# Kernel tuning notes

Measured on AMD Instinct MI355X. Metric: run time of the kernel, lower is better.

## Reference

```python
import jax, jax.numpy as jnp
import numpy as np

N_NODES = 50000
N_EDGES = 800000
IN_FEATS = 256
OUT_FEATS = 64


def setup_inputs() -> dict:
    key = jax.random.key(0)
    k1, k2, k3, k4 = jax.random.split(key, 4)
    feat = jax.random.normal(k1, (N_NODES, IN_FEATS), dtype=jnp.float32)
    src = jax.random.randint(k2, (N_EDGES,), 0, N_NODES, dtype=jnp.int32)
    dst = jax.random.randint(k3, (N_EDGES,), 0, N_NODES, dtype=jnp.int32)
    # Glorot-uniform like DGL's GraphConv weight init
    limit = float(np.sqrt(6.0 / (IN_FEATS + OUT_FEATS)))
    W = jax.random.uniform(k4, (IN_FEATS, OUT_FEATS), dtype=jnp.float32,
                           minval=-limit, maxval=limit)
    b = jnp.zeros((OUT_FEATS,), dtype=jnp.float32)
    return {"feat": feat, "src": src, "dst": dst, "W": W, "b": b}


def reference(feat, src, dst, W, b):
    n = feat.shape[0]
    ones = jnp.ones_like(src, dtype=feat.dtype)
    out_deg = jax.ops.segment_sum(ones, src, num_segments=n)
    in_deg = jax.ops.segment_sum(ones, dst, num_segments=n)
    # norm='both': deg^{-1/2}, degrees clamped to min 1 (allow_zero_in_degree)
    norm_src = jax.lax.rsqrt(jnp.maximum(out_deg, 1.0))   # [N]
    norm_dst = jax.lax.rsqrt(jnp.maximum(in_deg, 1.0))    # [N]
    # in_feats > out_feats -> apply weight before aggregation (DGL fast path)
    h = (feat * norm_src[:, None]) @ W                    # [N, out]
    agg = jax.ops.segment_sum(h[src], dst, num_segments=n)  # SpMM: sum messages at dst
    rst = agg * norm_dst[:, None] + b
    return jax.nn.sigmoid(rst)
```

## Files before the change

### kernel.cpp

```cpp
#include <hip/hip_runtime.h>
#include <hip/hip_bf16.h>
#include <math.h>

#define N_NODES 50000
#define N_EDGES 800000
#define IN_F 256
#define OUT_F 64

#define BKT 256
#define NB 196
#define CAP 6144
#define PARTA_BLOCKS 400
#define EPB (N_EDGES / PARTA_BLOCKS)
#define GEMM_BM 32
#define GEMM_BLOCKS 782

typedef __attribute__((ext_vector_type(8))) short bf16x8;
typedef __attribute__((ext_vector_type(4))) float f32x4;

__device__ __forceinline__ ushort f2bf(float x) {
    __hip_bfloat16 b = __float2bfloat16(x);
    return *reinterpret_cast<ushort*>(&b);
}
__device__ __forceinline__ float bf_lo(uint v) { return __uint_as_float(v << 16); }
__device__ __forceinline__ float bf_hi(uint v) { return __uint_as_float(v & 0xffff0000u); }

__global__ __launch_bounds__(256) void prep_kernel(int* __restrict__ bcnt,
                                                   const float* __restrict__ W,
                                                   ushort* __restrict__ Wpk) {
    const int tid = threadIdx.x;
    if (blockIdx.x == 0) {
        for (int i = tid; i < 2 * NB; i += 256) bcnt[i] = 0;
    } else {
        const int gid = (blockIdx.x - 1) * 256 + tid;
        const int lane = gid & 63;
        const int ct = (gid >> 6) & 3;
        const int step = gid >> 8;
        const int kg = lane >> 4;
        const int n = lane & 15;
        const float* base = W + (size_t)(step * 32 + kg * 8) * OUT_F + ct * 16 + n;
        union { ushort u[8]; uint4 v; } pk;
        #pragma unroll
        for (int j = 0; j < 8; ++j) pk.u[j] = f2bf(base[(size_t)j * OUT_F]);
        ((uint4*)Wpk)[gid] = pk.v;
    }
}

__global__ __launch_bounds__(512) void fused_kernel(const int* __restrict__ src,
                                                    const int* __restrict__ dst,
                                                    int* __restrict__ bcntD,
                                                    int* __restrict__ bcntS,
                                                    uint* __restrict__ pairsD,
                                                    ushort* __restrict__ srcloc,
                                                    const float* __restrict__ feat,
                                                    const ushort* __restrict__ Wpk,
                                                    ushort* __restrict__ h) {
    __shared__ __align__(16) char smem[65536];
    const int bi = blockIdx.x;
    const int tid = threadIdx.x;

    if (bi < 2 * PARTA_BLOCKS && (bi & 1)) {
        int2* ed      = (int2*)smem;
        uint* stgD    = (uint*)(smem + 16000);
        int* lcntD    = (int*)(smem + 24000);
        int* lcntS    = (int*)(smem + 25024);
        int* ldofD    = (int*)(smem + 26048);
        int* ldofS    = (int*)(smem + 27072);
        int* lbaseD   = (int*)(smem + 28096);
        int* lbaseS   = (int*)(smem + 28880);
        int* wtotD    = (int*)(smem + 29664);
        int* wtotS    = (int*)(smem + 29680);
        ushort* stgS  = (ushort*)(smem + 29696);
        const int id = bi >> 1;
        const int n4 = EPB / 4;

        for (int i = tid; i < 256; i += 512) { lcntD[i] = 0; lcntS[i] = 0; }
        __syncthreads();

        const int4* t4 = (const int4*)(dst + (size_t)id * EPB);
        const int4* s4 = (const int4*)(src + (size_t)id * EPB);
        for (int i = tid; i < n4; i += 512) {
            const int4 d = t4[i];
            const int4 s = s4[i];
            ed[4 * i + 0] = (int2){d.x, s.x};
            ed[4 * i + 1] = (int2){d.y, s.y};
            ed[4 * i + 2] = (int2){d.z, s.z};
            ed[4 * i + 3] = (int2){d.w, s.w};
            atomicAdd(&lcntD[d.x >> 8], 1); atomicAdd(&lcntS[s.x >> 8], 1);
            atomicAdd(&lcntD[d.y >> 8], 1); atomicAdd(&lcntS[s.y >> 8], 1);
            atomicAdd(&lcntD[d.z >> 8], 1); atomicAdd(&lcntS[s.z >> 8], 1);
            atomicAdd(&lcntD[d.w >> 8], 1); atomicAdd(&lcntS[s.w >> 8], 1);
        }
        __syncthreads();

        for (int i = tid; i < NB; i += 512) {
            const int cD = lcntD[i];
            lbaseD[i] = cD ? atomicAdd(&bcntD[i], cD) : 0;
            const int cS = lcntS[i];
            lbaseS[i] = cS ? atomicAdd(&bcntS[i], cS) : 0;
        }

        if (tid < 256) {
            const int lane = tid & 63;
            const int wave = tid >> 6;
            const int vD = lcntD[tid], vS = lcntS[tid];
            int iD = vD, iS = vS;
            #pragma unroll
            for (int d = 1; d < 64; d <<= 1) {
                const int uD = __shfl_up(iD, d, 64);
                const int uS = __shfl_up(iS, d, 64);
                if (lane >= d) { iD += uD; iS += uS; }
            }
            if (lane == 63) { wtotD[wave] = iD; wtotS[wave] = iS; }
            ldofD[tid] = iD - vD;
            ldofS[tid] = iS - vS;
        }
        __syncthreads();
        if (tid < 256) {
            const int wave = tid >> 6;
            int woD = 0, woS = 0;
            #pragma unroll
            for (int w = 0; w < 4; ++w)
                if (w < wave) { woD += wtotD[w]; woS += wtotS[w]; }
            ldofD[tid] += woD;
            ldofS[tid] += woS;
            lcntD[tid] = 0;
            lcntS[tid] = 0;
        }
        __syncthreads();

        for (int i = tid; i < EPB; i += 512) {
            const int2 e = ed[i];
            int bx = e.x >> 8;
            int pos = atomicAdd(&lcntD[bx], 1);
            stgD[ldofD[bx] + pos] =
                ((uint)bx << 24) | ((uint)(e.x & 255) << 16) | (uint)e.y;
            bx = e.y >> 8;
            pos = atomicAdd(&lcntS[bx], 1);
            stgS[ldofS[bx] + pos] = (ushort)((bx << 8) | (e.y & 255));
        }
        __syncthreads();

        for (int i = tid; i < EPB; i += 512) {
            const uint pv = stgD[i];
            const int bD = (int)(pv >> 24);
            pairsD[(size_t)bD * CAP + lbaseD[bD] + (i - ldofD[bD])] = pv & 0xFFFFFFu;
            const ushort sv = stgS[i];
            const int bS = sv >> 8;
            srcloc[(size_t)bS * CAP + lbaseS[bS] + (i - ldofS[bS])] = (ushort)(sv & 255u);
        }
    } else {
        const int id = (bi < 2 * PARTA_BLOCKS) ? (bi >> 1) : (bi - PARTA_BLOCKS);
        const int half = tid >> 8;
        const int t = tid & 255;
        const int lane = t & 63;
        const int wave = t >> 6;
        const int m = lane & 15;
        const int g = lane >> 4;
        const int rowBase = (id * 2 + half) * GEMM_BM;
        float* ftile = (float*)(smem + (size_t)half * 32768);
        const char* fb = (const char*)feat;

        #pragma unroll
        for (int it = 0; it < 8; ++it) {
            const int R = it * 4 + wave;
            const int off = (lane * 16) ^ ((R & 7) << 4);
            int grow = rowBase + R;
            if (grow >= N_NODES) grow = N_NODES - 1;
            __builtin_amdgcn_global_load_lds(
                (const __attribute__((address_space(1))) void*)(fb + ((size_t)grow << 10) + off),
                (__attribute__((address_space(3))) void*)((char*)ftile + it * 4096 + wave * 1024),
                16, 0, 0);
        }
        __syncthreads();

        const int rowHalf = wave & 1;
        const int colHalf = wave >> 1;

        f32x4 acc[2];
        acc[0] = (f32x4){0.f, 0.f, 0.f, 0.f};
        acc[1] = (f32x4){0.f, 0.f, 0.f, 0.f};

        const int Rr = rowHalf * 16 + m;
        const int swz = (Rr & 7) << 4;
        const char* rowb = (const char*)ftile + (Rr << 10);
        const bf16x8* wp = (const bf16x8*)Wpk;

        #pragma unroll
        for (int step = 0; step < 8; ++step) {
            const int kb = step * 128 + g * 32;
            const float4 a0 = *(const float4*)(rowb + (kb ^ swz));
            const float4 a1 = *(const float4*)(rowb + ((kb + 16) ^ swz));
            bf16x8 aa;
            aa[0] = (short)f2bf(a0.x); aa[1] = (short)f2bf(a0.y);
            aa[2] = (short)f2bf(a0.z); aa[3] = (short)f2bf(a0.w);
            aa[4] = (short)f2bf(a1.x); aa[5] = (short)f2bf(a1.y);
            aa[6] = (short)f2bf(a1.z); aa[7] = (short)f2bf(a1.w);
            #pragma unroll
            for (int ct = 0; ct < 2; ++ct)
                acc[ct] = __builtin_amdgcn_mfma_f32_16x16x32_bf16(
                    aa, wp[(step * 4 + colHalf * 2 + ct) * 64 + lane], acc[ct], 0, 0, 0);
        }

        #pragma unroll
        for (int j = 0; j < 4; ++j) {
            const int row = rowBase + rowHalf * 16 + g * 4 + j;
            if (row < N_NODES) {
                #pragma unroll
                for (int ct = 0; ct < 2; ++ct)
                    h[(size_t)row * OUT_F + colHalf * 32 + ct * 16 + m] = f2bf(acc[ct][j]);
            }
        }
    }
}

__global__ __launch_bounds__(1024) void bucket_kernel(const ushort* __restrict__ srcloc,
                                                      const int* __restrict__ bcntS,
                                                      float* __restrict__ normS,
                                                      const uint* __restrict__ pairsD,
                                                      const int* __restrict__ bcntD,
                                                      uint* __restrict__ ptrdeg,
                                                      ushort* __restrict__ sorted_src) {
    __shared__ int cnt[BKT];
    __shared__ int loff[BKT];
    __shared__ int wtot[4];
    const int bb = blockIdx.x;
    const int tid = threadIdx.x;
    const int node = bb * BKT + tid;

    if (tid < BKT) cnt[tid] = 0;
    __syncthreads();
    const int nS = bcntS[bb];
    const ushort* sp = srcloc + (size_t)bb * CAP;
    for (int i = tid; i < nS; i += 1024) atomicAdd(&cnt[sp[i]], 1);
    __syncthreads();
    if (tid < BKT && node < N_NODES)
        normS[node] = rsqrtf(fmaxf((float)cnt[tid], 1.0f));
    __syncthreads();

    if (tid < BKT) cnt[tid] = 0;
    __syncthreads();
    const int nD = bcntD[bb];
    const uint* pb = pairsD + (size_t)bb * CAP;
    for (int i = tid; i < nD; i += 1024) atomicAdd(&cnt[(pb[i] >> 16) & 255u], 1);
    __syncthreads();

    if (tid < BKT) {
        const int lane = tid & 63;
        const int wave = tid >> 6;
        const int v = cnt[tid];
        int incl = v;
        #pragma unroll
        for (int d = 1; d < 64; d <<= 1) {
            int u = __shfl_up(incl, d, 64);
            if (lane >= d) incl += u;
        }
        if (lane == 63) wtot[wave] = incl;
        loff[tid] = incl - v;
    }
    __syncthreads();
    if (tid < BKT) {
        const int wave = tid >> 6;
        int woff = 0;
        #pragma unroll
        for (int w = 0; w < 4; ++w)
            if (w < wave) woff += wtot[w];
        const int ex = woff + loff[tid];
        loff[tid] = ex;
        const int v = cnt[tid];
        cnt[tid] = 0;
        if (node < N_NODES)
            ptrdeg[node] = (uint)(bb * CAP + ex) | ((uint)v << 21);
    }
    __syncthreads();

    for (int i = tid; i < nD; i += 1024) {
        const uint p = pb[i];
        const int local = (int)((p >> 16) & 255u);
        const int pos = atomicAdd(&cnt[local], 1);
        sorted_src[(size_t)bb * CAP + loff[local] + pos] = (ushort)(p & 0xFFFFu);
    }
}

__global__ __launch_bounds__(256) void gather_kernel(const uint* __restrict__ ptrdeg,
                                                     const ushort* __restrict__ sorted_src,
                                                     const float* __restrict__ normS,
                                                     const ushort* __restrict__ h,
                                                     const float* __restrict__ b,
                                                     float* __restrict__ out) {
    const int lane = threadIdx.x & 63;
    const int q = lane & 15;
    const int g = lane >> 4;
    int nid = (int)((blockIdx.x * (size_t)blockDim.x + threadIdx.x) >> 6);
    if (nid >= N_NODES) return;
    nid = __builtin_amdgcn_readfirstlane(nid);

    const uint pd = ptrdeg[nid];
    const int beg = (int)(pd & 0x1FFFFFu);
    const int deg = (int)(pd >> 21);

    float a0 = 0.f, a1 = 0.f, a2 = 0.f, a3 = 0.f;
    const int nfull = deg >> 2;
    int e = beg + g;
    #pragma unroll 4
    for (int i = 0; i < nfull; ++i) {
        const int s = (int)sorted_src[e];
        e += 4;
        const float ns = normS[s];
        const uint2 v = *(const uint2*)(h + (size_t)s * OUT_F + q * 4);
        a0 = fmaf(ns, bf_lo(v.x), a0); a1 = fmaf(ns, bf_hi(v.x), a1);
        a2 = fmaf(ns, bf_lo(v.y), a2); a3 = fmaf(ns, bf_hi(v.y), a3);
    }
    const int rem = deg & 3;
    if (g < rem) {
        const int s = (int)sorted_src[beg + (deg & ~3) + g];
        const float ns = normS[s];
        const uint2 v = *(const uint2*)(h + (size_t)s * OUT_F + q * 4);
        a0 = fmaf(ns, bf_lo(v.x), a0); a1 = fmaf(ns, bf_hi(v.x), a1);
        a2 = fmaf(ns, bf_lo(v.y), a2); a3 = fmaf(ns, bf_hi(v.y), a3);
    }
    a0 += __shfl_xor(a0, 16, 64); a1 += __shfl_xor(a1, 16, 64);
    a2 += __shfl_xor(a2, 16, 64); a3 += __shfl_xor(a3, 16, 64);
    a0 += __shfl_xor(a0, 32, 64); a1 += __shfl_xor(a1, 32, 64);
    a2 += __shfl_xor(a2, 32, 64); a3 += __shfl_xor(a3, 32, 64);

    if (g == 0) {
        const float norm = rsqrtf(fmaxf((float)deg, 1.0f));
        const float4 bb = *(const float4*)(b + q * 4);
        float4 o;
        o.x = 1.0f / (1.0f + expf(-(a0 * norm + bb.x)));
        o.y = 1.0f / (1.0f + expf(-(a1 * norm + bb.y)));
        o.z = 1.0f / (1.0f + expf(-(a2 * norm + bb.z)));
        o.w = 1.0f / (1.0f + expf(-(a3 * norm + bb.w)));
        *(float4*)(out + (size_t)nid * OUT_F + q * 4) = o;
    }
}

extern "C" void kernel_launch(void* const* d_in, const int* in_sizes, int n_in,
                              void* d_out, int out_size, void* d_ws, size_t ws_size,
                              hipStream_t stream) {
    const float* feat = (const float*)d_in[0];
    const int* src    = (const int*)d_in[1];
    const int* dst    = (const int*)d_in[2];
    const float* W    = (const float*)d_in[3];
    const float* b    = (const float*)d_in[4];
    float* out = (float*)d_out;

    char* ws = (char*)d_ws;
    size_t off = 0;
    ushort* h = (ushort*)(ws + off);        off += (size_t)N_NODES * OUT_F * 2;
    float* normS = (float*)(ws + off);      off += (size_t)N_NODES * 4;
    uint* ptrdeg = (uint*)(ws + off);       off += (size_t)N_NODES * 4;
    int* bcnt = (int*)(ws + off);           off += (size_t)2 * NB * 4;
    ushort* Wpk = (ushort*)(ws + off);      off += (size_t)IN_F * OUT_F * 2;
    uint* pairsD = (uint*)(ws + off);       off += (size_t)NB * CAP * 4;
    ushort* srcloc = (ushort*)(ws + off);   off += (size_t)NB * CAP * 2;
    ushort* sorted_src = (ushort*)(ws + off); off += (size_t)NB * CAP * 2;
    int* bcntD = bcnt;
    int* bcntS = bcnt + NB;

    prep_kernel<<<9, 256, 0, stream>>>(bcnt, W, Wpk);

    fused_kernel<<<PARTA_BLOCKS + GEMM_BLOCKS, 512, 0, stream>>>(
        src, dst, bcntD, bcntS, pairsD, srcloc, feat, Wpk, h);

    bucket_kernel<<<NB, 1024, 0, stream>>>(srcloc, bcntS, normS,
                                           pairsD, bcntD, ptrdeg, sorted_src);

    gather_kernel<<<(N_NODES * 64 + 255) / 256, 256, 0, stream>>>(
        ptrdeg, sorted_src, normS, h, b, out);
}
```

Before: 68.15 us.

## Compute out-degree via LDS-chunked histogram instead of bucketing src edges

Removes the src-side bucket partition (srcloc scatter, local counts, scans) from the edge-partition blocks and replaces it with 64 dedicated histogram blocks. Each block counts one 12500-node range of src over a 1/16 slice of the edges in shared memory and atomically adds the nonzero counts to a global out-degree array, which bucket_kernel then reads directly to compute normS. This drops a scattered write plus re-read of 800K ushorts and halves the partition work, at the cost of each histogram block filtering its whole slice for in-range ids, extra global atomics, and a zeroing pass over the out-degree array.

```diff
diff --git a/kernel.cpp b/kernel.cpp
--- a/kernel.cpp
+++ b/kernel.cpp
@@ -14,6 +14,8 @@
 #define EPB (N_EDGES / PARTA_BLOCKS)
 #define GEMM_BM 32
 #define GEMM_BLOCKS 782
+#define HIST_CHUNK 12500
+#define HIST_BLOCKS 64
 
 typedef __attribute__((ext_vector_type(8))) short bf16x8;
 typedef __attribute__((ext_vector_type(4))) float f32x4;
@@ -25,13 +27,14 @@
 __device__ __forceinline__ float bf_lo(uint v) { return __uint_as_float(v << 16); }
 __device__ __forceinline__ float bf_hi(uint v) { return __uint_as_float(v & 0xffff0000u); }
 
-__global__ __launch_bounds__(256) void prep_kernel(int* __restrict__ bcnt,
+__global__ __launch_bounds__(256) void prep_kernel(int* __restrict__ bcntD,
                                                    const float* __restrict__ W,
-                                                   ushort* __restrict__ Wpk) {
+                                                   ushort* __restrict__ Wpk,
+                                                   int4* __restrict__ outdeg4) {
     const int tid = threadIdx.x;
     if (blockIdx.x == 0) {
-        for (int i = tid; i < 2 * NB; i += 256) bcnt[i] = 0;
-    } else {
+        for (int i = tid; i < NB; i += 256) bcntD[i] = 0;
+    } else if (blockIdx.x < 9) {
         const int gid = (blockIdx.x - 1) * 256 + tid;
         const int lane = gid & 63;
         const int ct = (gid >> 6) & 3;
@@ -43,15 +46,17 @@
         #pragma unroll
         for (int j = 0; j < 8; ++j) pk.u[j] = f2bf(base[(size_t)j * OUT_F]);
         ((uint4*)Wpk)[gid] = pk.v;
+    } else {
+        const int i = (blockIdx.x - 9) * 256 + tid;
+        if (i < N_NODES / 4) outdeg4[i] = (int4){0, 0, 0, 0};
     }
 }
 
 __global__ __launch_bounds__(512) void fused_kernel(const int* __restrict__ src,
                                                     const int* __restrict__ dst,
                                                     int* __restrict__ bcntD,
-                                                    int* __restrict__ bcntS,
                                                     uint* __restrict__ pairsD,
-                                                    ushort* __restrict__ srcloc,
+                                                    int* __restrict__ outdeg,
                                                     const float* __restrict__ feat,
                                                     const ushort* __restrict__ Wpk,
                                                     ushort* __restrict__ h) {
@@ -60,21 +65,16 @@
     const int tid = threadIdx.x;
 
     if (bi < 2 * PARTA_BLOCKS && (bi & 1)) {
-        int2* ed      = (int2*)smem;
-        uint* stgD    = (uint*)(smem + 16000);
-        int* lcntD    = (int*)(smem + 24000);
-        int* lcntS    = (int*)(smem + 25024);
-        int* ldofD    = (int*)(smem + 26048);
-        int* ldofS    = (int*)(smem + 27072);
-        int* lbaseD   = (int*)(smem + 28096);
-        int* lbaseS   = (int*)(smem + 28880);
-        int* wtotD    = (int*)(smem + 29664);
-        int* wtotS    = (int*)(smem + 29680);
-        ushort* stgS  = (ushort*)(smem + 29696);
+        int2* ed    = (int2*)smem;
+        uint* stgD  = (uint*)(smem + 16000);
+        int* lcntD  = (int*)(smem + 24000);
+        int* ldofD  = (int*)(smem + 25024);
+        int* lbaseD = (int*)(smem + 26048);
+        int* wtotD  = (int*)(smem + 26832);
         const int id = bi >> 1;
         const int n4 = EPB / 4;
 
-        for (int i = tid; i < 256; i += 512) { lcntD[i] = 0; lcntS[i] = 0; }
+        for (int i = tid; i < 256; i += 512) lcntD[i] = 0;
         __syncthreads();
 
         const int4* t4 = (const int4*)(dst + (size_t)id * EPB);
@@ -86,58 +86,49 @@
             ed[4 * i + 1] = (int2){d.y, s.y};
             ed[4 * i + 2] = (int2){d.z, s.z};
             ed[4 * i + 3] = (int2){d.w, s.w};
-            atomicAdd(&lcntD[d.x >> 8], 1); atomicAdd(&lcntS[s.x >> 8], 1);
-            atomicAdd(&lcntD[d.y >> 8], 1); atomicAdd(&lcntS[s.y >> 8], 1);
-            atomicAdd(&lcntD[d.z >> 8], 1); atomicAdd(&lcntS[s.z >> 8], 1);
-            atomicAdd(&lcntD[d.w >> 8], 1); atomicAdd(&lcntS[s.w >> 8], 1);
+            atomicAdd(&lcntD[d.x >> 8], 1);
+            atomicAdd(&lcntD[d.y >> 8], 1);
+            atomicAdd(&lcntD[d.z >> 8], 1);
+            atomicAdd(&lcntD[d.w >> 8], 1);
         }
         __syncthreads();
 
         for (int i = tid; i < NB; i += 512) {
             const int cD = lcntD[i];
             lbaseD[i] = cD ? atomicAdd(&bcntD[i], cD) : 0;
-            const int cS = lcntS[i];
-            lbaseS[i] = cS ? atomicAdd(&bcntS[i], cS) : 0;
         }
 
         if (tid < 256) {
             const int lane = tid & 63;
             const int wave = tid >> 6;
-            const int vD = lcntD[tid], vS = lcntS[tid];
-            int iD = vD, iS = vS;
+            const int vD = lcntD[tid];
+            int iD = vD;
             #pragma unroll
             for (int d = 1; d < 64; d <<= 1) {
                 const int uD = __shfl_up(iD, d, 64);
-                const int uS = __shfl_up(iS, d, 64);
-                if (lane >= d) { iD += uD; iS += uS; }
+                if (lane >= d) iD += uD;
             }
-            if (lane == 63) { wtotD[wave] = iD; wtotS[wave] = iS; }
+            if (lane == 63) wtotD[wave] = iD;
             ldofD[tid] = iD - vD;
-            ldofS[tid] = iS - vS;
         }
         __syncthreads();
         if (tid < 256) {
             const int wave = tid >> 6;
-            int woD = 0, woS = 0;
+            int woD = 0;
             #pragma unroll
             for (int w = 0; w < 4; ++w)
-                if (w < wave) { woD += wtotD[w]; woS += wtotS[w]; }
+                if (w < wave) woD += wtotD[w];
             ldofD[tid] += woD;
-            ldofS[tid] += woS;
             lcntD[tid] = 0;
-            lcntS[tid] = 0;
         }
         __syncthreads();
 
         for (int i = tid; i < EPB; i += 512) {
             const int2 e = ed[i];
-            int bx = e.x >> 8;
-            int pos = atomicAdd(&lcntD[bx], 1);
+            const int bx = e.x >> 8;
+            const int pos = atomicAdd(&lcntD[bx], 1);
             stgD[ldofD[bx] + pos] =
                 ((uint)bx << 24) | ((uint)(e.x & 255) << 16) | (uint)e.y;
-            bx = e.y >> 8;
-            pos = atomicAdd(&lcntS[bx], 1);
-            stgS[ldofS[bx] + pos] = (ushort)((bx << 8) | (e.y & 255));
         }
         __syncthreads();
 
@@ -145,12 +136,38 @@
             const uint pv = stgD[i];
             const int bD = (int)(pv >> 24);
             pairsD[(size_t)bD * CAP + lbaseD[bD] + (i - ldofD[bD])] = pv & 0xFFFFFFu;
-            const ushort sv = stgS[i];
-            const int bS = sv >> 8;
-            srcloc[(size_t)bS * CAP + lbaseS[bS] + (i - ldofS[bS])] = (ushort)(sv & 255u);
+        }
+    } else if (bi >= 2 * PARTA_BLOCKS && bi < 2 * PARTA_BLOCKS + 2 * HIST_BLOCKS
+               && (bi & 1)) {
+        int* cnt = (int*)smem;
+        const int id = (bi - 2 * PARTA_BLOCKS) >> 1;
+        const int chunk = id >> 4;
+        const int slice = id & 15;
+        const int base = chunk * HIST_CHUNK;
+
+        for (int i = tid; i < HIST_CHUNK; i += 512) cnt[i] = 0;
+        __syncthreads();
+
+        const int4* s4 = (const int4*)(src + (size_t)slice * (N_EDGES / 16));
+        for (int i = tid; i < (N_EDGES / 16) / 4; i += 512) {
+            const int4 v = s4[i];
+            int r;
+            r = v.x - base; if ((unsigned)r < (unsigned)HIST_CHUNK) atomicAdd(&cnt[r], 1);
+            r = v.y - base; if ((unsigned)r < (unsigned)HIST_CHUNK) atomicAdd(&cnt[r], 1);
+            r = v.z - base; if ((unsigned)r < (unsigned)HIST_CHUNK) atomicAdd(&cnt[r], 1);
+            r = v.w - base; if ((unsigned)r < (unsigned)HIST_CHUNK) atomicAdd(&cnt[r], 1);
+        }
+        __syncthreads();
+
+        for (int i = tid; i < HIST_CHUNK; i += 512) {
+            const int c = cnt[i];
+            if (c) atomicAdd(&outdeg[base + i], c);
         }
     } else {
-        const int id = (bi < 2 * PARTA_BLOCKS) ? (bi >> 1) : (bi - PARTA_BLOCKS);
+        const int id = (bi < 2 * PARTA_BLOCKS) ? (bi >> 1)
+                     : (bi < 2 * PARTA_BLOCKS + 2 * HIST_BLOCKS)
+                         ? (PARTA_BLOCKS + ((bi - 2 * PARTA_BLOCKS) >> 1))
+                         : (bi - PARTA_BLOCKS - HIST_BLOCKS);
         const int half = tid >> 8;
         const int t = tid & 255;
         const int lane = t & 63;
@@ -214,8 +231,7 @@
     }
 }
 
-__global__ __launch_bounds__(1024) void bucket_kernel(const ushort* __restrict__ srcloc,
-                                                      const int* __restrict__ bcntS,
+__global__ __launch_bounds__(1024) void bucket_kernel(const int* __restrict__ outdeg,
                                                       float* __restrict__ normS,
                                                       const uint* __restrict__ pairsD,
                                                       const int* __restrict__ bcntD,
@@ -228,17 +244,11 @@
     const int tid = threadIdx.x;
     const int node = bb * BKT + tid;
 
-    if (tid < BKT) cnt[tid] = 0;
-    __syncthreads();
-    const int nS = bcntS[bb];
-    const ushort* sp = srcloc + (size_t)bb * CAP;
-    for (int i = tid; i < nS; i += 1024) atomicAdd(&cnt[sp[i]], 1);
-    __syncthreads();
-    if (tid < BKT && node < N_NODES)
-        normS[node] = rsqrtf(fmaxf((float)cnt[tid], 1.0f));
-    __syncthreads();
-
-    if (tid < BKT) cnt[tid] = 0;
+    if (tid < BKT) {
+        cnt[tid] = 0;
+        if (node < N_NODES)
+            normS[node] = rsqrtf(fmaxf((float)outdeg[node], 1.0f));
+    }
     __syncthreads();
     const int nD = bcntD[bb];
     const uint* pb = pairsD + (size_t)bb * CAP;
@@ -351,20 +361,19 @@
     ushort* h = (ushort*)(ws + off);        off += (size_t)N_NODES * OUT_F * 2;
     float* normS = (float*)(ws + off);      off += (size_t)N_NODES * 4;
     uint* ptrdeg = (uint*)(ws + off);       off += (size_t)N_NODES * 4;
-    int* bcnt = (int*)(ws + off);           off += (size_t)2 * NB * 4;
+    int* outdeg = (int*)(ws + off);         off += (size_t)N_NODES * 4;
+    int* bcntD = (int*)(ws + off);          off += (size_t)NB * 4 + 16;
     ushort* Wpk = (ushort*)(ws + off);      off += (size_t)IN_F * OUT_F * 2;
     uint* pairsD = (uint*)(ws + off);       off += (size_t)NB * CAP * 4;
-    ushort* srcloc = (ushort*)(ws + off);   off += (size_t)NB * CAP * 2;
     ushort* sorted_src = (ushort*)(ws + off); off += (size_t)NB * CAP * 2;
-    int* bcntD = bcnt;
-    int* bcntS = bcnt + NB;
-
-    prep_kernel<<<9, 256, 0, stream>>>(bcnt, W, Wpk);
-
-    fused_kernel<<<PARTA_BLOCKS + GEMM_BLOCKS, 512, 0, stream>>>(
-        src, dst, bcntD, bcntS, pairsD, srcloc, feat, Wpk, h);
-
-    bucket_kernel<<<NB, 1024, 0, stream>>>(srcloc, bcntS, normS,
+
+    prep_kernel<<<9 + (N_NODES / 4 + 255) / 256, 256, 0, stream>>>(
+        bcntD, W, Wpk, (int4*)outdeg);
+
+    fused_kernel<<<PARTA_BLOCKS + HIST_BLOCKS + GEMM_BLOCKS, 512, 0, stream>>>(
+        src, dst, bcntD, pairsD, outdeg, feat, Wpk, h);
+
+    bucket_kernel<<<NB, 1024, 0, stream>>>(outdeg, normS,
                                            pairsD, bcntD, ptrdeg, sorted_src);
 
     gather_kernel<<<(N_NODES * 64 + 255) / 256, 256, 0, stream>>>(
```

After: 68.03 us. Within noise of the previous version (-0.2%).
